# Optimization experiments

Hardware: AMD Instinct MI355X
Metric: run time of the kernel (lower is better)

Reference implementation:

```python
import jax, jax.numpy as jnp
import numpy as np
from jax import lax

N, H, BS = 256, 1024, 128
ALPHA, BETA, SIGMA = 60.0, 20.0, 5.0
EPS = 1e-8


def _mlp_w(key, n_in, n_out):
    return jax.random.normal(key, (n_out, n_in), dtype=jnp.float32) / np.sqrt(n_in)


def setup_inputs() -> dict:
    key = jax.random.key(0)
    ks = jax.random.split(key, 8)
    inp = {
        "t": jnp.zeros((), dtype=jnp.float32),
        "x": jax.random.normal(ks[0], (BS, N), dtype=jnp.float32),
        "Wf1": _mlp_w(ks[1], N, H), "bf1": jnp.zeros((H,), jnp.float32),
        "Wf2": _mlp_w(ks[2], H, N), "bf2": jnp.zeros((N,), jnp.float32),
        "Wg1": _mlp_w(ks[3], N, H), "bg1": jnp.zeros((H,), jnp.float32),
        "Wg2": _mlp_w(ks[4], H, N), "bg2": jnp.zeros((N,), jnp.float32),
        "Wk1": _mlp_w(ks[5], N, H), "bk1": jnp.zeros((H,), jnp.float32),
        "Wk2": _mlp_w(ks[6], H, N), "bk2": jnp.zeros((N,), jnp.float32),
    }
    return inp


def reference(t, x, Wf1, bf1, Wf2, bf2, Wg1, bg1, Wg2, bg2, Wk1, bk1, Wk2, bk2):
    def mlp(u, W1, b1, W2, b2):
        return jnp.tanh(u @ W1.T + b1) @ W2.T + b2

    def k_func(u):
        return mlp(u, Wk1, bk1, Wk2, bk2)

    f_out = mlp(x, Wf1, bf1, Wf2, bf2)          # f_model(t, x); t unused
    k_out = k_func(x)
    G_k_out = mlp(x, Wg1, bg1, Wg2, bg2)        # g_fn(x)[0]
    dx_dt = f_out + G_k_out

    # compute_k_jacobian: torch detaches u, so no grad flows to x here.
    # torch layout: J[b, j, i] = d k_i / d u_j  (transpose of jacfwd output)
    x_d = lax.stop_gradient(x)
    J_fwd = jax.vmap(jax.jacfwd(k_func))(x_d)   # [bs, i_out, j_in]
    J_x = jnp.swapaxes(J_fwd, 1, 2)             # [bs, j, i]

    k_norm = jnp.linalg.norm(k_out, axis=1)                      # [bs]
    Jf = jnp.einsum('bji,bi->bj', J_x, f_out)                    # bmm(J, f)
    Jf_norm = jnp.linalg.norm(Jf, axis=1)
    c1 = Jf_norm - ALPHA * k_norm ** (2 * SIGMA - 1)
    JG = jnp.einsum('bji,bi->bj', J_x, G_k_out)                  # bmm(J, G)
    c2 = jnp.sum(k_out * JG, axis=1) - BETA * k_norm ** (2 * SIGMA)

    mask = (c1 > EPS) | (c2 < -EPS)                              # [bs]
    dx_upd = jnp.where(mask[:, None], jnp.zeros_like(dx_dt), dx_dt)
    return (dx_upd + dx_dt) / 2
```

## Files before the change

### kernel.cpp

```cpp
#include <hip/hip_runtime.h>
#include <stdint.h>

#define N_ 256
#define H_ 1024
#define BS_ 128

#define WS_SK    0
#define WS_OACC  131072
#define WS_OPART 229376
#define WS_JPART 1802240
#define WS_FLOATS 2850816

__global__ __launch_bounds__(512) void k12_l1l2(
    const float* __restrict__ x,
    const float* __restrict__ Wf1, const float* __restrict__ bf1,
    const float* __restrict__ Wg1, const float* __restrict__ bg1,
    const float* __restrict__ Wk1, const float* __restrict__ bk1,
    const float* __restrict__ Wf2, const float* __restrict__ bf2,
    const float* __restrict__ Wg2, const float* __restrict__ bg2,
    const float* __restrict__ Wk2, const float* __restrict__ bk2,
    float* __restrict__ sk, float* __restrict__ opart)
{
    const int bx = blockIdx.x;
    const int g  = bx % 48;
    const int rt = bx / 48;
    const int m  = g >> 4;
    const int ht = g & 15;
    const int t  = threadIdx.x;
    const int h0 = ht * 64;
    const int r0 = rt * 16;

    const float* W1 = (m == 0) ? Wf1 : (m == 1) ? Wg1 : Wk1;
    const float* b1 = (m == 0) ? bf1 : (m == 1) ? bg1 : bk1;
    const float* W2 = (m == 0) ? Wf2 : (m == 1) ? Wg2 : Wk2;
    const float* b2 = (m == 0) ? bf2 : (m == 1) ? bg2 : bk2;

    __shared__ __align__(16) float xs[16][256];
    __shared__ __align__(16) float ts[16][64];
    for (int u = t; u < 1024; u += 512)
        ((float4*)xs)[u] = ((const float4*)(x + r0 * N_))[u];
    __syncthreads();

    {
        const int hl = t & 63;
        const int rq = (t >> 6) * 2;
        const int h  = h0 + hl;
        float a0 = b1[h], a1 = a0;
        const float4* w4 = (const float4*)(W1 + h * N_);
        const float4* x0 = (const float4*)xs[rq];
        const float4* x1 = (const float4*)xs[rq + 1];
        #pragma unroll 8
        for (int c = 0; c < 64; ++c) {
            float4 w = w4[c];
            float4 p = x0[c];
            a0 += w.x * p.x + w.y * p.y + w.z * p.z + w.w * p.w;
            float4 q = x1[c];
            a1 += w.x * q.x + w.y * q.y + w.z * q.z + w.w * q.w;
        }
        const float v0 = tanhf(a0), v1 = tanhf(a1);
        ts[rq][hl] = v0; ts[rq + 1][hl] = v1;
        if (m == 2) {
            sk[(r0 + rq) * H_ + h]     = 1.0f - v0 * v0;
            sk[(r0 + rq + 1) * H_ + h] = 1.0f - v1 * v1;
        }
    }
    __syncthreads();

    {
        const int i  = t & 255;
        const int hf = (t >> 8) * 8;
        float acc[8];
        const float bv = (ht == 0) ? b2[i] : 0.0f;
        #pragma unroll
        for (int r = 0; r < 8; ++r) acc[r] = bv;

        const float4* w4 = (const float4*)(W2 + i * H_ + h0);
        #pragma unroll 2
        for (int c = 0; c < 16; ++c) {
            float4 w = w4[c];
            #pragma unroll
            for (int r = 0; r < 8; ++r) {
                float4 a = ((const float4*)ts[hf + r])[c];
                acc[r] += w.x * a.x + w.y * a.y + w.z * a.z + w.w * a.w;
            }
        }
        #pragma unroll
        for (int r = 0; r < 8; ++r)
            opart[((ht * 3 + m) * BS_ + r0 + hf + r) * N_ + i] = acc[r];
    }
}

__global__ __launch_bounds__(256) void k25_reduce(
    const float* __restrict__ opart, float* __restrict__ oacc)
{
    const int tid = blockIdx.x * 256 + threadIdx.x;
    float s = 0.f;
    #pragma unroll
    for (int ks = 0; ks < 16; ++ks)
        s += opart[ks * (3 * BS_ * N_) + tid];
    oacc[tid] = s;
}

__global__ __launch_bounds__(256) void k3_vj(
    const float* __restrict__ Wk1, const float* __restrict__ Wk2,
    const float* __restrict__ oacc, const float* __restrict__ sk,
    float* __restrict__ jpart)
{
    const int q  = blockIdx.x & 15;
    const int rp = blockIdx.x >> 4;
    const int t  = threadIdx.x;
    const int r0 = rp * 4;
    const int h0 = q * 64;

    __shared__ float fos[4][256], gos[4][256];
    __shared__ float sfv[4][64], sgv[4][64];

    for (int u = t; u < 1024; u += 256) {
        const int r = u >> 8, i = u & 255;
        fos[r][i] = oacc[(r0 + r) * N_ + i];
        gos[r][i] = oacc[(BS_ + r0 + r) * N_ + i];
    }
    __syncthreads();

    {
        const int hl = t & 63;
        const int rl = t >> 6;
        const int h  = h0 + hl;
        const float* w2 = Wk2 + h;
        float vf = 0.f, vg = 0.f;
        #pragma unroll 8
        for (int c = 0; c < 64; ++c) {
            const float4 of = ((const float4*)fos[rl])[c];
            const float4 og = ((const float4*)gos[rl])[c];
            const float w0 = w2[(4 * c + 0) * H_];
            const float w1 = w2[(4 * c + 1) * H_];
            const float w2v = w2[(4 * c + 2) * H_];
            const float w3 = w2[(4 * c + 3) * H_];
            vf += of.x * w0 + of.y * w1 + of.z * w2v + of.w * w3;
            vg += og.x * w0 + og.y * w1 + og.z * w2v + og.w * w3;
        }
        const float s = sk[(r0 + rl) * H_ + h];
        sfv[rl][hl] = s * vf;
        sgv[rl][hl] = s * vg;
    }
    __syncthreads();

    {
        float jf[4] = {0.f, 0.f, 0.f, 0.f};
        float jg[4] = {0.f, 0.f, 0.f, 0.f};
        const float* w1 = Wk1 + h0 * N_ + t;
        #pragma unroll 4
        for (int c = 0; c < 16; ++c) {
            const float w0 = w1[(4 * c + 0) * N_];
            const float wv1 = w1[(4 * c + 1) * N_];
            const float wv2 = w1[(4 * c + 2) * N_];
            const float wv3 = w1[(4 * c + 3) * N_];
            #pragma unroll
            for (int r = 0; r < 4; ++r) {
                const float4 sf = ((const float4*)sfv[r])[c];
                const float4 sg = ((const float4*)sgv[r])[c];
                jf[r] += sf.x * w0 + sf.y * wv1 + sf.z * wv2 + sf.w * wv3;
                jg[r] += sg.x * w0 + sg.y * wv1 + sg.z * wv2 + sg.w * wv3;
            }
        }
        #pragma unroll
        for (int r = 0; r < 4; ++r) {
            jpart[((q * 2 + 0) * BS_ + r0 + r) * N_ + t] = jf[r];
            jpart[((q * 2 + 1) * BS_ + r0 + r) * N_ + t] = jg[r];
        }
    }
}

__global__ __launch_bounds__(256) void k4_final(
    const float* __restrict__ oacc,
    const float* __restrict__ jpart,
    float* __restrict__ out)
{
    const int r = blockIdx.x;
    const int t = threadIdx.x;
    __shared__ float red[12];

    const float fo = oacc[r * N_ + t];
    const float go = oacc[(BS_ + r) * N_ + t];
    const float ko = oacc[(2 * BS_ + r) * N_ + t];

    float jf = 0.f, jg = 0.f;
    #pragma unroll
    for (int q = 0; q < 16; ++q) {
        jf += jpart[((q * 2 + 0) * BS_ + r) * N_ + t];
        jg += jpart[((q * 2 + 1) * BS_ + r) * N_ + t];
    }

    float v0 = ko * ko, v1 = jf * jf, v2 = ko * jg;
    #pragma unroll
    for (int o = 32; o > 0; o >>= 1) {
        v0 += __shfl_xor(v0, o, 64);
        v1 += __shfl_xor(v1, o, 64);
        v2 += __shfl_xor(v2, o, 64);
    }
    const int wid = t >> 6;
    if ((t & 63) == 0) {
        red[wid * 3 + 0] = v0;
        red[wid * 3 + 1] = v1;
        red[wid * 3 + 2] = v2;
    }
    __syncthreads();
    const float kn2 = red[0] + red[3] + red[6] + red[9];
    const float jf2 = red[1] + red[4] + red[7] + red[10];
    const float kjg = red[2] + red[5] + red[8] + red[11];

    const float knorm = sqrtf(kn2);
    const float kn4 = kn2 * kn2;
    const float kn8 = kn4 * kn4;
    const float c1 = sqrtf(jf2) - 60.0f * kn8 * knorm;
    const float c2 = kjg - 20.0f * kn8 * kn2;
    const float scale = ((c1 > 1e-8f) || (c2 < -1e-8f)) ? 0.5f : 1.0f;

    out[r * N_ + t] = (fo + go) * scale;
}

__global__ __launch_bounds__(256) void manifold_fused(
    const float* __restrict__ x,
    const float* __restrict__ Wf1, const float* __restrict__ bf1v,
    const float* __restrict__ Wf2, const float* __restrict__ bf2v,
    const float* __restrict__ Wg1, const float* __restrict__ bg1v,
    const float* __restrict__ Wg2, const float* __restrict__ bg2v,
    const float* __restrict__ Wk1, const float* __restrict__ bk1v,
    const float* __restrict__ Wk2, const float* __restrict__ bk2v,
    float* __restrict__ out)
{
    const int b = blockIdx.x;
    const int t = threadIdx.x;
    __shared__ float xs[N_];
    __shared__ float tf[H_], tg[H_], tk[H_], sk[H_];
    __shared__ float fo[N_], go[N_];
    __shared__ float sfv[H_], sgv[H_];
    __shared__ float red[12];

    xs[t] = x[b * N_ + t];
    __syncthreads();
    {
        float acc[12];
        const float4* rows[12];
        #pragma unroll
        for (int m = 0; m < 4; ++m) {
            const int h = t + m * 256;
            rows[m]     = (const float4*)(Wf1 + h * N_);
            rows[4 + m] = (const float4*)(Wg1 + h * N_);
            rows[8 + m] = (const float4*)(Wk1 + h * N_);
            acc[m] = bf1v[h]; acc[4 + m] = bg1v[h]; acc[8 + m] = bk1v[h];
        }
        const float4* xs4 = (const float4*)xs;
        #pragma unroll 2
        for (int c = 0; c < 64; ++c) {
            float4 a = xs4[c];
            #pragma unroll
            for (int r = 0; r < 12; ++r) {
                float4 w = rows[r][c];
                acc[r] += w.x * a.x + w.y * a.y + w.z * a.z + w.w * a.w;
            }
        }
        #pragma unroll
        for (int m = 0; m < 4; ++m) {
            const int h = t + m * 256;
            float vtf = tanhf(acc[m]);
            float vtg = tanhf(acc[4 + m]);
            float vtk = tanhf(acc[8 + m]);
            tf[h] = vtf; tg[h] = vtg; tk[h] = vtk; sk[h] = 1.0f - vtk * vtk;
        }
    }
    __syncthreads();
    float af = bf2v[t], ag = bg2v[t], ak = bk2v[t];
    {
        const float4* rf = (const float4*)(Wf2 + t * H_);
        const float4* rg = (const float4*)(Wg2 + t * H_);
        const float4* rk = (const float4*)(Wk2 + t * H_);
        #pragma unroll 2
        for (int c = 0; c < 256; ++c) {
            float4 wf = rf[c], wg = rg[c], wk = rk[c];
            float4 vf = ((const float4*)tf)[c];
            af += wf.x*vf.x + wf.y*vf.y + wf.z*vf.z + wf.w*vf.w;
            float4 vg = ((const float4*)tg)[c];
            ag += wg.x*vg.x + wg.y*vg.y + wg.z*vg.z + wg.w*vg.w;
            float4 vk = ((const float4*)tk)[c];
            ak += wk.x*vk.x + wk.y*vk.y + wk.z*vk.z + wk.w*vk.w;
        }
    }
    fo[t] = af; go[t] = ag;
    __syncthreads();
    {
        float vf[4] = {0.f,0.f,0.f,0.f}, vg[4] = {0.f,0.f,0.f,0.f};
        const float* base = Wk2 + 4 * t;
        #pragma unroll 4
        for (int i = 0; i < N_; ++i) {
            float4 w = *(const float4*)(base + i * H_);
            float fv = fo[i], gv = go[i];
            vf[0]+=w.x*fv; vf[1]+=w.y*fv; vf[2]+=w.z*fv; vf[3]+=w.w*fv;
            vg[0]+=w.x*gv; vg[1]+=w.y*gv; vg[2]+=w.z*gv; vg[3]+=w.w*gv;
        }
        #pragma unroll
        for (int c = 0; c < 4; ++c) {
            sfv[4*t+c] = sk[4*t+c]*vf[c];
            sgv[4*t+c] = sk[4*t+c]*vg[c];
        }
    }
    __syncthreads();
    float jf = 0.f, jg = 0.f;
    {
        const float* col = Wk1 + t;
        #pragma unroll 4
        for (int c = 0; c < 256; ++c) {
            float4 s4 = ((const float4*)sfv)[c];
            float4 g4 = ((const float4*)sgv)[c];
            const int h = c * 4;
            float w0 = col[(h+0)*N_], w1 = col[(h+1)*N_];
            float w2 = col[(h+2)*N_], w3 = col[(h+3)*N_];
            jf += s4.x*w0 + s4.y*w1 + s4.z*w2 + s4.w*w3;
            jg += g4.x*w0 + g4.y*w1 + g4.z*w2 + g4.w*w3;
        }
    }
    float v0 = ak*ak, v1 = jf*jf, v2 = ak*jg;
    #pragma unroll
    for (int o = 32; o > 0; o >>= 1) {
        v0 += __shfl_xor(v0, o, 64);
        v1 += __shfl_xor(v1, o, 64);
        v2 += __shfl_xor(v2, o, 64);
    }
    const int wid = t >> 6;
    if ((t & 63) == 0) {
        red[wid*3+0] = v0; red[wid*3+1] = v1; red[wid*3+2] = v2;
    }
    __syncthreads();
    const float kn2 = red[0]+red[3]+red[6]+red[9];
    const float jf2 = red[1]+red[4]+red[7]+red[10];
    const float kjg = red[2]+red[5]+red[8]+red[11];
    const float knorm = sqrtf(kn2);
    const float kn4 = kn2*kn2, kn8 = kn4*kn4;
    const float c1 = sqrtf(jf2) - 60.0f*kn8*knorm;
    const float c2 = kjg - 20.0f*kn8*kn2;
    const float scale = ((c1 > 1e-8f) || (c2 < -1e-8f)) ? 0.5f : 1.0f;
    out[b*N_+t] = (af+ag)*scale;
}

extern "C" void kernel_launch(void* const* d_in, const int* in_sizes, int n_in,
                              void* d_out, int out_size, void* d_ws, size_t ws_size,
                              hipStream_t stream) {
    const float* x    = (const float*)d_in[1];
    const float* Wf1  = (const float*)d_in[2];
    const float* bf1v = (const float*)d_in[3];
    const float* Wf2  = (const float*)d_in[4];
    const float* bf2v = (const float*)d_in[5];
    const float* Wg1  = (const float*)d_in[6];
    const float* bg1v = (const float*)d_in[7];
    const float* Wg2  = (const float*)d_in[8];
    const float* bg2v = (const float*)d_in[9];
    const float* Wk1  = (const float*)d_in[10];
    const float* bk1v = (const float*)d_in[11];
    const float* Wk2  = (const float*)d_in[12];
    const float* bk2v = (const float*)d_in[13];
    float* out = (float*)d_out;

    if (ws_size < (size_t)WS_FLOATS * sizeof(float)) {
        manifold_fused<<<BS_, 256, 0, stream>>>(
            x, Wf1, bf1v, Wf2, bf2v, Wg1, bg1v, Wg2, bg2v,
            Wk1, bk1v, Wk2, bk2v, out);
        return;
    }

    float* ws    = (float*)d_ws;
    float* sk    = ws + WS_SK;
    float* oacc  = ws + WS_OACC;
    float* opart = ws + WS_OPART;
    float* jpart = ws + WS_JPART;

    k12_l1l2  <<<384, 512, 0, stream>>>(x, Wf1, bf1v, Wg1, bg1v, Wk1, bk1v,
                                        Wf2, bf2v, Wg2, bg2v, Wk2, bk2v,
                                        sk, opart);
    k25_reduce<<<384, 256, 0, stream>>>(opart, oacc);
    k3_vj     <<<512, 256, 0, stream>>>(Wk1, Wk2, oacc, sk, jpart);
    k4_final  <<<BS_, 256, 0, stream>>>(oacc, jpart, out);
}
```

Before: 139.7 us.

## Split fused layer-1/layer-2 kernel into two finer-grained kernels with swizzled LDS weight tiles

Replaces the single fused first/second-layer kernel with two kernels: one computes the tanh hidden activations for all three MLPs and stores them in workspace (reusing the jpart region), and the other computes the second-layer partial sums. Each kernel uses 1536 small 128-thread blocks that stage a weight tile in XOR-swizzled shared memory to avoid bank conflicts, and remaps block ids to spread work across XCDs. Layer 1 splits the K dimension across lanes and reduces with shuffles. This raises parallelism and weight reuse from LDS, at the cost of an extra launch and a global round trip for the hidden activations.

```diff
diff --git a/kernel.cpp b/kernel.cpp
--- a/kernel.cpp
+++ b/kernel.cpp
@@ -11,83 +11,126 @@
 #define WS_JPART 1802240
 #define WS_FLOATS 2850816
 
-__global__ __launch_bounds__(512) void k12_l1l2(
+__global__ __launch_bounds__(128) void k1_l1(
     const float* __restrict__ x,
     const float* __restrict__ Wf1, const float* __restrict__ bf1,
     const float* __restrict__ Wg1, const float* __restrict__ bg1,
     const float* __restrict__ Wk1, const float* __restrict__ bk1,
+    float* __restrict__ tg, float* __restrict__ sk)
+{
+    const int bx  = blockIdx.x;
+    const int sid = (bx & 7) * 192 + (bx >> 3);
+    const int g   = sid >> 4;
+    const int rt  = sid & 15;
+    const int m   = g >> 5;
+    const int ht  = g & 31;
+    const int h0  = ht * 32;
+    const int r0  = rt * 8;
+
+    const float* W1 = (m == 0) ? Wf1 : (m == 1) ? Wg1 : Wk1;
+    const float* b1 = (m == 0) ? bf1 : (m == 1) ? bg1 : bk1;
+
+    __shared__ float4 ws4[32 * 64];
+
+    const int t = threadIdx.x;
+    {
+        const float4* wg = (const float4*)(W1 + h0 * N_);
+        #pragma unroll
+        for (int v = 0; v < 16; ++v) {
+            const int f4  = t + 128 * v;
+            const int row = f4 >> 6, c = f4 & 63;
+            ws4[(row << 6) | (c & 48) | ((c & 15) ^ (row & 15))] = wg[f4];
+        }
+    }
+    __syncthreads();
+
+    const int l  = t & 63;
+    const int w  = t >> 6;
+    const int hl = l & 15;
+    const int kq = l >> 4;
+    const int h  = h0 + w * 16 + hl;
+
+    float acc[8] = {0.f,0.f,0.f,0.f,0.f,0.f,0.f,0.f};
+    const float4* wrow = ws4 + ((w * 16 + hl) << 6) + (kq << 4);
+    const float4* xg   = (const float4*)(x + r0 * N_) + (kq << 4);
+    #pragma unroll 4
+    for (int c = 0; c < 16; ++c) {
+        const float4 wv = wrow[c ^ hl];
+        #pragma unroll
+        for (int r = 0; r < 8; ++r) {
+            const float4 xv = xg[(r << 6) + c];
+            acc[r] += wv.x*xv.x + wv.y*xv.y + wv.z*xv.z + wv.w*xv.w;
+        }
+    }
+    #pragma unroll
+    for (int r = 0; r < 8; ++r) {
+        acc[r] += __shfl_xor(acc[r], 16, 64);
+        acc[r] += __shfl_xor(acc[r], 32, 64);
+    }
+    const float bv = b1[h];
+    const int ra = kq * 2, rb = ra + 1;
+    const float va = tanhf(acc[ra] + bv);
+    const float vb = tanhf(acc[rb] + bv);
+    tg[(m * BS_ + r0 + ra) * H_ + h] = va;
+    tg[(m * BS_ + r0 + rb) * H_ + h] = vb;
+    if (m == 2) {
+        sk[(r0 + ra) * H_ + h] = 1.0f - va * va;
+        sk[(r0 + rb) * H_ + h] = 1.0f - vb * vb;
+    }
+}
+
+__global__ __launch_bounds__(128) void k2_l2(
+    const float* __restrict__ tg,
     const float* __restrict__ Wf2, const float* __restrict__ bf2,
     const float* __restrict__ Wg2, const float* __restrict__ bg2,
     const float* __restrict__ Wk2, const float* __restrict__ bk2,
-    float* __restrict__ sk, float* __restrict__ opart)
-{
-    const int bx = blockIdx.x;
-    const int g  = bx % 48;
-    const int rt = bx / 48;
-    const int m  = g >> 4;
-    const int ht = g & 15;
-    const int t  = threadIdx.x;
-    const int h0 = ht * 64;
-    const int r0 = rt * 16;
-
-    const float* W1 = (m == 0) ? Wf1 : (m == 1) ? Wg1 : Wk1;
-    const float* b1 = (m == 0) ? bf1 : (m == 1) ? bg1 : bk1;
+    float* __restrict__ opart)
+{
+    const int bx  = blockIdx.x;
+    const int sid = (bx & 7) * 192 + (bx >> 3);
+    const int g   = sid >> 4;
+    const int rt  = sid & 15;
+    const int m   = g >> 5;
+    const int ks  = (g >> 1) & 15;
+    const int ih  = g & 1;
+    const int r0  = rt * 8;
+    const int k0  = ks * 64;
+    const int i0  = ih * 128;
+
     const float* W2 = (m == 0) ? Wf2 : (m == 1) ? Wg2 : Wk2;
     const float* b2 = (m == 0) ? bf2 : (m == 1) ? bg2 : bk2;
 
-    __shared__ __align__(16) float xs[16][256];
-    __shared__ __align__(16) float ts[16][64];
-    for (int u = t; u < 1024; u += 512)
-        ((float4*)xs)[u] = ((const float4*)(x + r0 * N_))[u];
-    __syncthreads();
-
-    {
-        const int hl = t & 63;
-        const int rq = (t >> 6) * 2;
-        const int h  = h0 + hl;
-        float a0 = b1[h], a1 = a0;
-        const float4* w4 = (const float4*)(W1 + h * N_);
-        const float4* x0 = (const float4*)xs[rq];
-        const float4* x1 = (const float4*)xs[rq + 1];
-        #pragma unroll 8
-        for (int c = 0; c < 64; ++c) {
-            float4 w = w4[c];
-            float4 p = x0[c];
-            a0 += w.x * p.x + w.y * p.y + w.z * p.z + w.w * p.w;
-            float4 q = x1[c];
-            a1 += w.x * q.x + w.y * q.y + w.z * q.z + w.w * q.w;
-        }
-        const float v0 = tanhf(a0), v1 = tanhf(a1);
-        ts[rq][hl] = v0; ts[rq + 1][hl] = v1;
-        if (m == 2) {
-            sk[(r0 + rq) * H_ + h]     = 1.0f - v0 * v0;
-            sk[(r0 + rq + 1) * H_ + h] = 1.0f - v1 * v1;
-        }
-    }
-    __syncthreads();
-
-    {
-        const int i  = t & 255;
-        const int hf = (t >> 8) * 8;
-        float acc[8];
-        const float bv = (ht == 0) ? b2[i] : 0.0f;
-        #pragma unroll
-        for (int r = 0; r < 8; ++r) acc[r] = bv;
-
-        const float4* w4 = (const float4*)(W2 + i * H_ + h0);
-        #pragma unroll 2
-        for (int c = 0; c < 16; ++c) {
-            float4 w = w4[c];
-            #pragma unroll
-            for (int r = 0; r < 8; ++r) {
-                float4 a = ((const float4*)ts[hf + r])[c];
-                acc[r] += w.x * a.x + w.y * a.y + w.z * a.z + w.w * a.w;
-            }
-        }
-        #pragma unroll
-        for (int r = 0; r < 8; ++r)
-            opart[((ht * 3 + m) * BS_ + r0 + hf + r) * N_ + i] = acc[r];
-    }
+    __shared__ float4 w2s[128 * 16];
+
+    const int t = threadIdx.x;
+    {
+        #pragma unroll
+        for (int v = 0; v < 16; ++v) {
+            const int row = (t >> 4) + (v << 3);
+            const int c   = t & 15;
+            const float4 wv = ((const float4*)(W2 + (i0 + row) * H_ + k0))[c];
+            w2s[(row << 4) | (c ^ (row & 15))] = wv;
+        }
+    }
+    __syncthreads();
+
+    const int i = i0 + t;
+    float acc[8] = {0.f,0.f,0.f,0.f,0.f,0.f,0.f,0.f};
+    const float4* wrow = w2s + (t << 4);
+    const float4* trow = (const float4*)(tg + (m * BS_ + r0) * H_ + k0);
+    #pragma unroll 4
+    for (int c = 0; c < 16; ++c) {
+        const float4 wv = wrow[c ^ (t & 15)];
+        #pragma unroll
+        for (int r = 0; r < 8; ++r) {
+            const float4 tv = trow[(r << 8) + c];
+            acc[r] += wv.x*tv.x + wv.y*tv.y + wv.z*tv.z + wv.w*tv.w;
+        }
+    }
+    const float bv = (ks == 0) ? b2[i] : 0.0f;
+    #pragma unroll
+    for (int r = 0; r < 8; ++r)
+        opart[((ks * 3 + m) * BS_ + r0 + r) * N_ + i] = acc[r] + bv;
 }
 
 __global__ __launch_bounds__(256) void k25_reduce(
@@ -372,10 +415,12 @@
     float* oacc  = ws + WS_OACC;
     float* opart = ws + WS_OPART;
     float* jpart = ws + WS_JPART;
-
-    k12_l1l2  <<<384, 512, 0, stream>>>(x, Wf1, bf1v, Wg1, bg1v, Wk1, bk1v,
-                                        Wf2, bf2v, Wg2, bg2v, Wk2, bk2v,
-                                        sk, opart);
+    float* tg    = ws + WS_JPART;
+
+    k1_l1     <<<1536, 128, 0, stream>>>(x, Wf1, bf1v, Wg1, bg1v, Wk1, bk1v,
+                                         tg, sk);
+    k2_l2     <<<1536, 128, 0, stream>>>(tg, Wf2, bf2v, Wg2, bg2v, Wk2, bk2v,
+                                         opart);
     k25_reduce<<<384, 256, 0, stream>>>(opart, oacc);
     k3_vj     <<<512, 256, 0, stream>>>(Wk1, Wk2, oacc, sk, jpart);
     k4_final  <<<BS_, 256, 0, stream>>>(oacc, jpart, out);
```

Result: slower. 143.3 us (+2.6%).

## Merge four kernels into one persistent kernel with software grid barriers

Applied to the files above, without the earlier changes.

Replaces the four-launch pipeline (layer1+layer2, reduce, vector-Jacobian, final) with a single 512-block persistent kernel that separates the phases with atomic-counter grid barriers. Layer 1 and layer 2 become separate phases with swizzled LDS weight tiles and the hidden activations staged in global memory. The reduce kernel is removed by summing the partials where they are consumed. This is meant to cut launch gaps and inter-kernel idle time. It adds a memset launch and spin-wait barriers that assume all 512 blocks are co-resident, which risks deadlock if they are not.

```diff
diff --git a/kernel.cpp b/kernel.cpp
--- a/kernel.cpp
+++ b/kernel.cpp
@@ -6,12 +6,27 @@
 #define BS_ 128
 
 #define WS_SK    0
-#define WS_OACC  131072
+#define WS_BAR   131072
 #define WS_OPART 229376
 #define WS_JPART 1802240
 #define WS_FLOATS 2850816
 
-__global__ __launch_bounds__(512) void k12_l1l2(
+#define GRID_ 512
+
+__device__ __forceinline__ void grid_barrier(int* cnt) {
+    __syncthreads();
+    if (threadIdx.x == 0) {
+        __threadfence();
+        atomicAdd(cnt, 1);
+        while (__hip_atomic_load(cnt, __ATOMIC_RELAXED,
+                                 __HIP_MEMORY_SCOPE_AGENT) < GRID_)
+            __builtin_amdgcn_s_sleep(2);
+    }
+    __syncthreads();
+    __threadfence();
+}
+
+__global__ __launch_bounds__(256, 2) void mega(
     const float* __restrict__ x,
     const float* __restrict__ Wf1, const float* __restrict__ bf1,
     const float* __restrict__ Wg1, const float* __restrict__ bg1,
@@ -19,204 +34,232 @@
     const float* __restrict__ Wf2, const float* __restrict__ bf2,
     const float* __restrict__ Wg2, const float* __restrict__ bg2,
     const float* __restrict__ Wk2, const float* __restrict__ bk2,
-    float* __restrict__ sk, float* __restrict__ opart)
+    float* __restrict__ ws, float* __restrict__ out)
 {
-    const int bx = blockIdx.x;
-    const int g  = bx % 48;
-    const int rt = bx / 48;
-    const int m  = g >> 4;
-    const int ht = g & 15;
-    const int t  = threadIdx.x;
-    const int h0 = ht * 64;
-    const int r0 = rt * 16;
-
-    const float* W1 = (m == 0) ? Wf1 : (m == 1) ? Wg1 : Wk1;
-    const float* b1 = (m == 0) ? bf1 : (m == 1) ? bg1 : bk1;
-    const float* W2 = (m == 0) ? Wf2 : (m == 1) ? Wg2 : Wk2;
-    const float* b2 = (m == 0) ? bf2 : (m == 1) ? bg2 : bk2;
-
-    __shared__ __align__(16) float xs[16][256];
-    __shared__ __align__(16) float ts[16][64];
-    for (int u = t; u < 1024; u += 512)
-        ((float4*)xs)[u] = ((const float4*)(x + r0 * N_))[u];
-    __syncthreads();
-
-    {
-        const int hl = t & 63;
-        const int rq = (t >> 6) * 2;
-        const int h  = h0 + hl;
-        float a0 = b1[h], a1 = a0;
-        const float4* w4 = (const float4*)(W1 + h * N_);
-        const float4* x0 = (const float4*)xs[rq];
-        const float4* x1 = (const float4*)xs[rq + 1];
-        #pragma unroll 8
-        for (int c = 0; c < 64; ++c) {
-            float4 w = w4[c];
-            float4 p = x0[c];
-            a0 += w.x * p.x + w.y * p.y + w.z * p.z + w.w * p.w;
-            float4 q = x1[c];
-            a1 += w.x * q.x + w.y * q.y + w.z * q.z + w.w * q.w;
-        }
-        const float v0 = tanhf(a0), v1 = tanhf(a1);
-        ts[rq][hl] = v0; ts[rq + 1][hl] = v1;
-        if (m == 2) {
-            sk[(r0 + rq) * H_ + h]     = 1.0f - v0 * v0;
-            sk[(r0 + rq + 1) * H_ + h] = 1.0f - v1 * v1;
-        }
-    }
-    __syncthreads();
-
-    {
-        const int i  = t & 255;
-        const int hf = (t >> 8) * 8;
-        float acc[8];
-        const float bv = (ht == 0) ? b2[i] : 0.0f;
-        #pragma unroll
-        for (int r = 0; r < 8; ++r) acc[r] = bv;
-
-        const float4* w4 = (const float4*)(W2 + i * H_ + h0);
-        #pragma unroll 2
-        for (int c = 0; c < 16; ++c) {
-            float4 w = w4[c];
-            #pragma unroll
-            for (int r = 0; r < 8; ++r) {
-                float4 a = ((const float4*)ts[hf + r])[c];
-                acc[r] += w.x * a.x + w.y * a.y + w.z * a.z + w.w * a.w;
-            }
-        }
-        #pragma unroll
-        for (int r = 0; r < 8; ++r)
-            opart[((ht * 3 + m) * BS_ + r0 + hf + r) * N_ + i] = acc[r];
-    }
-}
-
-__global__ __launch_bounds__(256) void k25_reduce(
-    const float* __restrict__ opart, float* __restrict__ oacc)
-{
-    const int tid = blockIdx.x * 256 + threadIdx.x;
-    float s = 0.f;
-    #pragma unroll
-    for (int ks = 0; ks < 16; ++ks)
-        s += opart[ks * (3 * BS_ * N_) + tid];
-    oacc[tid] = s;
-}
-
-__global__ __launch_bounds__(256) void k3_vj(
-    const float* __restrict__ Wk1, const float* __restrict__ Wk2,
-    const float* __restrict__ oacc, const float* __restrict__ sk,
-    float* __restrict__ jpart)
-{
-    const int q  = blockIdx.x & 15;
-    const int rp = blockIdx.x >> 4;
-    const int t  = threadIdx.x;
-    const int r0 = rp * 4;
-    const int h0 = q * 64;
-
-    __shared__ float fos[4][256], gos[4][256];
-    __shared__ float sfv[4][64], sgv[4][64];
-
-    for (int u = t; u < 1024; u += 256) {
-        const int r = u >> 8, i = u & 255;
-        fos[r][i] = oacc[(r0 + r) * N_ + i];
-        gos[r][i] = oacc[(BS_ + r0 + r) * N_ + i];
-    }
-    __syncthreads();
-
-    {
-        const int hl = t & 63;
-        const int rl = t >> 6;
-        const int h  = h0 + hl;
-        const float* w2 = Wk2 + h;
-        float vf = 0.f, vg = 0.f;
-        #pragma unroll 8
-        for (int c = 0; c < 64; ++c) {
-            const float4 of = ((const float4*)fos[rl])[c];
-            const float4 og = ((const float4*)gos[rl])[c];
-            const float w0 = w2[(4 * c + 0) * H_];
-            const float w1 = w2[(4 * c + 1) * H_];
-            const float w2v = w2[(4 * c + 2) * H_];
-            const float w3 = w2[(4 * c + 3) * H_];
-            vf += of.x * w0 + of.y * w1 + of.z * w2v + of.w * w3;
-            vg += og.x * w0 + og.y * w1 + og.z * w2v + og.w * w3;
-        }
-        const float s = sk[(r0 + rl) * H_ + h];
-        sfv[rl][hl] = s * vf;
-        sgv[rl][hl] = s * vg;
-    }
-    __syncthreads();
-
-    {
-        float jf[4] = {0.f, 0.f, 0.f, 0.f};
-        float jg[4] = {0.f, 0.f, 0.f, 0.f};
-        const float* w1 = Wk1 + h0 * N_ + t;
+    const int bid = blockIdx.x;
+    const int t   = threadIdx.x;
+
+    float* skw   = ws + WS_SK;
+    int*   bar   = (int*)(ws + WS_BAR);
+    float* opart = ws + WS_OPART;
+    float* jpart = ws + WS_JPART;
+    float* tg    = ws + WS_JPART;
+
+    __shared__ __align__(16) float smem[8192];
+    __shared__ float red[12];
+    float4* sm4 = (float4*)smem;
+
+    for (int u = bid; u < 1536; u += GRID_) {
+        const int m  = u >> 9;
+        const int r9 = u & 511;
+        const int ht = r9 >> 4;
+        const int rt = r9 & 15;
+        const int h0 = ht * 32, r0 = rt * 8;
+
+        const float* W1 = (m == 0) ? Wf1 : (m == 1) ? Wg1 : Wk1;
+        const float* b1 = (m == 0) ? bf1 : (m == 1) ? bg1 : bk1;
+
+        __syncthreads();
+        const float4* wg = (const float4*)(W1 + h0 * N_);
+        #pragma unroll
+        for (int v = 0; v < 8; ++v) {
+            const int f4  = t + 256 * v;
+            const int row = f4 >> 6, c = f4 & 63;
+            sm4[(row << 6) | (c & 48) | ((c & 15) ^ (row & 15))] = wg[f4];
+        }
+        __syncthreads();
+
+        const int hl = t & 15;
+        const int kq = (t >> 4) & 3;
+        const int w2i = (t >> 6) & 1;
+        const int rh = t >> 7;
+        const int hloc = w2i * 16 + hl;
+        const int h = h0 + hloc;
+
+        float acc[4] = {0.f, 0.f, 0.f, 0.f};
+        const float4* wrow = sm4 + (hloc << 6) + (kq << 4);
+        const float4* xg   = (const float4*)(x + (r0 + rh * 4) * N_) + (kq << 4);
         #pragma unroll 4
         for (int c = 0; c < 16; ++c) {
-            const float w0 = w1[(4 * c + 0) * N_];
-            const float wv1 = w1[(4 * c + 1) * N_];
-            const float wv2 = w1[(4 * c + 2) * N_];
-            const float wv3 = w1[(4 * c + 3) * N_];
+            const float4 wv = wrow[c ^ hl];
+            #pragma unroll
+            for (int j = 0; j < 4; ++j) {
+                const float4 xv = xg[(j << 6) + c];
+                acc[j] += wv.x*xv.x + wv.y*xv.y + wv.z*xv.z + wv.w*xv.w;
+            }
+        }
+        #pragma unroll
+        for (int j = 0; j < 4; ++j) {
+            acc[j] += __shfl_xor(acc[j], 16, 64);
+            acc[j] += __shfl_xor(acc[j], 32, 64);
+        }
+        float av = acc[0];
+        av = (kq == 1) ? acc[1] : av;
+        av = (kq == 2) ? acc[2] : av;
+        av = (kq == 3) ? acc[3] : av;
+        const float v0 = tanhf(av + b1[h]);
+        const int r = r0 + rh * 4 + kq;
+        tg[(m * BS_ + r) * H_ + h] = v0;
+        if (m == 2) skw[r * H_ + h] = 1.0f - v0 * v0;
+    }
+    grid_barrier(bar + 0);
+
+    for (int u = bid; u < 1536; u += GRID_) {
+        const int m  = u >> 9;
+        const int ks = (u >> 5) & 15;
+        const int ih = (u >> 4) & 1;
+        const int rt = u & 15;
+        const int k0 = ks * 64, i0 = ih * 128, r0 = rt * 8;
+
+        const float* W2 = (m == 0) ? Wf2 : (m == 1) ? Wg2 : Wk2;
+        const float* b2 = (m == 0) ? bf2 : (m == 1) ? bg2 : bk2;
+
+        __syncthreads();
+        #pragma unroll
+        for (int v = 0; v < 8; ++v) {
+            const int idx = t + 256 * v;
+            const int row = idx >> 4, c = idx & 15;
+            sm4[(row << 4) | (c ^ (row & 15))] =
+                ((const float4*)(W2 + (i0 + row) * H_ + k0))[c];
+        }
+        __syncthreads();
+
+        const int i  = t & 127;
+        const int rh = t >> 7;
+        float acc[4] = {0.f, 0.f, 0.f, 0.f};
+        const float4* wrow = sm4 + (i << 4);
+        const float4* trow = (const float4*)(tg + (m * BS_ + r0 + rh * 4) * H_ + k0);
+        #pragma unroll 4
+        for (int c = 0; c < 16; ++c) {
+            const float4 wv = wrow[c ^ (i & 15)];
+            #pragma unroll
+            for (int j = 0; j < 4; ++j) {
+                const float4 tv = trow[(j << 8) + c];
+                acc[j] += wv.x*tv.x + wv.y*tv.y + wv.z*tv.z + wv.w*tv.w;
+            }
+        }
+        const float bv = (ks == 0) ? b2[i0 + i] : 0.0f;
+        #pragma unroll
+        for (int j = 0; j < 4; ++j)
+            opart[((ks * 3 + m) * BS_ + r0 + rh * 4 + j) * N_ + i0 + i] = acc[j] + bv;
+    }
+    grid_barrier(bar + 1);
+
+    {
+        const int q  = bid & 15;
+        const int rp = bid >> 4;
+        const int r0 = rp * 4, h0 = q * 64;
+
+        float (*fos)[256] = (float(*)[256])smem;
+        float (*gos)[256] = (float(*)[256])(smem + 1024);
+        float (*sfv)[64]  = (float(*)[64])(smem + 2048);
+        float (*sgv)[64]  = (float(*)[64])(smem + 2304);
+
+        for (int u2 = t; u2 < 1024; u2 += 256) {
+            const int r = u2 >> 8, i = u2 & 255;
+            float sf = 0.f, sg = 0.f;
+            #pragma unroll
+            for (int ks2 = 0; ks2 < 16; ++ks2) {
+                sf += opart[((ks2 * 3 + 0) * BS_ + r0 + r) * N_ + i];
+                sg += opart[((ks2 * 3 + 1) * BS_ + r0 + r) * N_ + i];
+            }
+            fos[r][i] = sf; gos[r][i] = sg;
+        }
+        __syncthreads();
+
+        {
+            const int hl = t & 63;
+            const int rl = t >> 6;
+            const int h  = h0 + hl;
+            const float* w2 = Wk2 + h;
+            float vf = 0.f, vg = 0.f;
+            #pragma unroll 8
+            for (int c = 0; c < 64; ++c) {
+                const float4 of = ((const float4*)fos[rl])[c];
+                const float4 og = ((const float4*)gos[rl])[c];
+                const float w0  = w2[(4 * c + 0) * H_];
+                const float w1v = w2[(4 * c + 1) * H_];
+                const float w2v = w2[(4 * c + 2) * H_];
+                const float w3  = w2[(4 * c + 3) * H_];
+                vf += of.x * w0 + of.y * w1v + of.z * w2v + of.w * w3;
+                vg += og.x * w0 + og.y * w1v + og.z * w2v + og.w * w3;
+            }
+            const float s = skw[(r0 + rl) * H_ + h];
+            sfv[rl][hl] = s * vf;
+            sgv[rl][hl] = s * vg;
+        }
+        __syncthreads();
+
+        {
+            float jf[4] = {0.f, 0.f, 0.f, 0.f};
+            float jg[4] = {0.f, 0.f, 0.f, 0.f};
+            const float* w1 = Wk1 + h0 * N_ + t;
+            #pragma unroll 4
+            for (int c = 0; c < 16; ++c) {
+                const float w0  = w1[(4 * c + 0) * N_];
+                const float wv1 = w1[(4 * c + 1) * N_];
+                const float wv2 = w1[(4 * c + 2) * N_];
+                const float wv3 = w1[(4 * c + 3) * N_];
+                #pragma unroll
+                for (int r = 0; r < 4; ++r) {
+                    const float4 sf = ((const float4*)sfv[r])[c];
+                    const float4 sg = ((const float4*)sgv[r])[c];
+                    jf[r] += sf.x * w0 + sf.y * wv1 + sf.z * wv2 + sf.w * wv3;
+                    jg[r] += sg.x * w0 + sg.y * wv1 + sg.z * wv2 + sg.w * wv3;
+                }
+            }
             #pragma unroll
             for (int r = 0; r < 4; ++r) {
-                const float4 sf = ((const float4*)sfv[r])[c];
-                const float4 sg = ((const float4*)sgv[r])[c];
-                jf[r] += sf.x * w0 + sf.y * wv1 + sf.z * wv2 + sf.w * wv3;
-                jg[r] += sg.x * w0 + sg.y * wv1 + sg.z * wv2 + sg.w * wv3;
-            }
-        }
-        #pragma unroll
-        for (int r = 0; r < 4; ++r) {
-            jpart[((q * 2 + 0) * BS_ + r0 + r) * N_ + t] = jf[r];
-            jpart[((q * 2 + 1) * BS_ + r0 + r) * N_ + t] = jg[r];
-        }
-    }
-}
-
-__global__ __launch_bounds__(256) void k4_final(
-    const float* __restrict__ oacc,
-    const float* __restrict__ jpart,
-    float* __restrict__ out)
-{
-    const int r = blockIdx.x;
-    const int t = threadIdx.x;
-    __shared__ float red[12];
-
-    const float fo = oacc[r * N_ + t];
-    const float go = oacc[(BS_ + r) * N_ + t];
-    const float ko = oacc[(2 * BS_ + r) * N_ + t];
-
-    float jf = 0.f, jg = 0.f;
-    #pragma unroll
-    for (int q = 0; q < 16; ++q) {
-        jf += jpart[((q * 2 + 0) * BS_ + r) * N_ + t];
-        jg += jpart[((q * 2 + 1) * BS_ + r) * N_ + t];
-    }
-
-    float v0 = ko * ko, v1 = jf * jf, v2 = ko * jg;
-    #pragma unroll
-    for (int o = 32; o > 0; o >>= 1) {
-        v0 += __shfl_xor(v0, o, 64);
-        v1 += __shfl_xor(v1, o, 64);
-        v2 += __shfl_xor(v2, o, 64);
-    }
-    const int wid = t >> 6;
-    if ((t & 63) == 0) {
-        red[wid * 3 + 0] = v0;
-        red[wid * 3 + 1] = v1;
-        red[wid * 3 + 2] = v2;
-    }
-    __syncthreads();
-    const float kn2 = red[0] + red[3] + red[6] + red[9];
-    const float jf2 = red[1] + red[4] + red[7] + red[10];
-    const float kjg = red[2] + red[5] + red[8] + red[11];
-
-    const float knorm = sqrtf(kn2);
-    const float kn4 = kn2 * kn2;
-    const float kn8 = kn4 * kn4;
-    const float c1 = sqrtf(jf2) - 60.0f * kn8 * knorm;
-    const float c2 = kjg - 20.0f * kn8 * kn2;
-    const float scale = ((c1 > 1e-8f) || (c2 < -1e-8f)) ? 0.5f : 1.0f;
-
-    out[r * N_ + t] = (fo + go) * scale;
+                jpart[((q * 2 + 0) * BS_ + r0 + r) * N_ + t] = jf[r];
+                jpart[((q * 2 + 1) * BS_ + r0 + r) * N_ + t] = jg[r];
+            }
+        }
+    }
+    grid_barrier(bar + 2);
+
+    if (bid < BS_) {
+        const int r = bid;
+        float fo = 0.f, go = 0.f, ko = 0.f;
+        #pragma unroll
+        for (int ks2 = 0; ks2 < 16; ++ks2) {
+            fo += opart[((ks2 * 3 + 0) * BS_ + r) * N_ + t];
+            go += opart[((ks2 * 3 + 1) * BS_ + r) * N_ + t];
+            ko += opart[((ks2 * 3 + 2) * BS_ + r) * N_ + t];
+        }
+        float jf = 0.f, jg = 0.f;
+        #pragma unroll
+        for (int q2 = 0; q2 < 16; ++q2) {
+            jf += jpart[((q2 * 2 + 0) * BS_ + r) * N_ + t];
+            jg += jpart[((q2 * 2 + 1) * BS_ + r) * N_ + t];
+        }
+
+        float v0 = ko * ko, v1 = jf * jf, v2 = ko * jg;
+        #pragma unroll
+        for (int o = 32; o > 0; o >>= 1) {
+            v0 += __shfl_xor(v0, o, 64);
+            v1 += __shfl_xor(v1, o, 64);
+            v2 += __shfl_xor(v2, o, 64);
+        }
+        const int wid = t >> 6;
+        if ((t & 63) == 0) {
+            red[wid * 3 + 0] = v0;
+            red[wid * 3 + 1] = v1;
+            red[wid * 3 + 2] = v2;
+        }
+        __syncthreads();
+        const float kn2 = red[0] + red[3] + red[6] + red[9];
+        const float jf2 = red[1] + red[4] + red[7] + red[10];
+        const float kjg = red[2] + red[5] + red[8] + red[11];
+
+        const float knorm = sqrtf(kn2);
+        const float kn4 = kn2 * kn2;
+        const float kn8 = kn4 * kn4;
+        const float c1 = sqrtf(jf2) - 60.0f * kn8 * knorm;
+        const float c2 = kjg - 20.0f * kn8 * kn2;
+        const float scale = ((c1 > 1e-8f) || (c2 < -1e-8f)) ? 0.5f : 1.0f;
+
+        out[r * N_ + t] = (fo + go) * scale;
+    }
 }
 
 __global__ __launch_bounds__(256) void manifold_fused(
@@ -367,16 +410,10 @@
         return;
     }
 
-    float* ws    = (float*)d_ws;
-    float* sk    = ws + WS_SK;
-    float* oacc  = ws + WS_OACC;
-    float* opart = ws + WS_OPART;
-    float* jpart = ws + WS_JPART;
-
-    k12_l1l2  <<<384, 512, 0, stream>>>(x, Wf1, bf1v, Wg1, bg1v, Wk1, bk1v,
-                                        Wf2, bf2v, Wg2, bg2v, Wk2, bk2v,
-                                        sk, opart);
-    k25_reduce<<<384, 256, 0, stream>>>(opart, oacc);
-    k3_vj     <<<512, 256, 0, stream>>>(Wk1, Wk2, oacc, sk, jpart);
-    k4_final  <<<BS_, 256, 0, stream>>>(oacc, jpart, out);
+    float* ws = (float*)d_ws;
+    hipMemsetAsync(ws + WS_BAR, 0, 64, stream);
+    mega<<<GRID_, 256, 0, stream>>>(
+        x, Wf1, bf1v, Wg1, bg1v, Wk1, bk1v,
+        Wf2, bf2v, Wg2, bg2v, Wk2, bk2v,
+        ws, out);
 }
```

Result: slower. 351.7 us (+151.8%).

## Stage MLP weights in swizzled shared memory with finer hidden tiles in fused layer kernel

Applied to the files above, without the earlier changes.

The fused layer-1/layer-2 kernel now uses 768 blocks of 256 threads, each covering 32 hidden units instead of 64. It stages W1 and W2 tiles into XOR-swizzled LDS so the weights are read coalesced from global memory instead of through strided per-thread row loads. Layer 1 splits the K dimension across lanes and reduces with shuffles, and block IDs are remapped so neighbouring blocks spread across XCDs. The cost is twice as many partial sums (32 slices) for the reduce kernel to read and a larger workspace.

```diff
diff --git a/kernel.cpp b/kernel.cpp
--- a/kernel.cpp
+++ b/kernel.cpp
@@ -8,10 +8,10 @@
 #define WS_SK    0
 #define WS_OACC  131072
 #define WS_OPART 229376
-#define WS_JPART 1802240
-#define WS_FLOATS 2850816
-
-__global__ __launch_bounds__(512) void k12_l1l2(
+#define WS_JPART 3375104
+#define WS_FLOATS 4423680
+
+__global__ __launch_bounds__(256) void k12s(
     const float* __restrict__ x,
     const float* __restrict__ Wf1, const float* __restrict__ bf1,
     const float* __restrict__ Wg1, const float* __restrict__ bg1,
@@ -21,72 +21,110 @@
     const float* __restrict__ Wk2, const float* __restrict__ bk2,
     float* __restrict__ sk, float* __restrict__ opart)
 {
-    const int bx = blockIdx.x;
-    const int g  = bx % 48;
-    const int rt = bx / 48;
-    const int m  = g >> 4;
-    const int ht = g & 15;
-    const int t  = threadIdx.x;
-    const int h0 = ht * 64;
-    const int r0 = rt * 16;
+    const int bx  = blockIdx.x;
+    const int sid = (bx & 7) * 96 + (bx >> 3);
+    const int g   = sid >> 3;
+    const int rt  = sid & 7;
+    const int m   = g >> 5;
+    const int ht  = g & 31;
+    const int t   = threadIdx.x;
+    const int h0  = ht * 32;
+    const int r0  = rt * 16;
 
     const float* W1 = (m == 0) ? Wf1 : (m == 1) ? Wg1 : Wk1;
     const float* b1 = (m == 0) ? bf1 : (m == 1) ? bg1 : bk1;
     const float* W2 = (m == 0) ? Wf2 : (m == 1) ? Wg2 : Wk2;
     const float* b2 = (m == 0) ? bf2 : (m == 1) ? bg2 : bk2;
 
+    __shared__ float4 wbuf[2048];
     __shared__ __align__(16) float xs[16][256];
-    __shared__ __align__(16) float ts[16][64];
-    for (int u = t; u < 1024; u += 512)
-        ((float4*)xs)[u] = ((const float4*)(x + r0 * N_))[u];
-    __syncthreads();
-
-    {
-        const int hl = t & 63;
-        const int rq = (t >> 6) * 2;
-        const int h  = h0 + hl;
-        float a0 = b1[h], a1 = a0;
-        const float4* w4 = (const float4*)(W1 + h * N_);
-        const float4* x0 = (const float4*)xs[rq];
-        const float4* x1 = (const float4*)xs[rq + 1];
-        #pragma unroll 8
-        for (int c = 0; c < 64; ++c) {
-            float4 w = w4[c];
-            float4 p = x0[c];
-            a0 += w.x * p.x + w.y * p.y + w.z * p.z + w.w * p.w;
-            float4 q = x1[c];
-            a1 += w.x * q.x + w.y * q.y + w.z * q.z + w.w * q.w;
-        }
-        const float v0 = tanhf(a0), v1 = tanhf(a1);
-        ts[rq][hl] = v0; ts[rq + 1][hl] = v1;
-        if (m == 2) {
-            sk[(r0 + rq) * H_ + h]     = 1.0f - v0 * v0;
-            sk[(r0 + rq + 1) * H_ + h] = 1.0f - v1 * v1;
-        }
-    }
-    __syncthreads();
-
-    {
-        const int i  = t & 255;
-        const int hf = (t >> 8) * 8;
-        float acc[8];
-        const float bv = (ht == 0) ? b2[i] : 0.0f;
-        #pragma unroll
-        for (int r = 0; r < 8; ++r) acc[r] = bv;
-
-        const float4* w4 = (const float4*)(W2 + i * H_ + h0);
-        #pragma unroll 2
-        for (int c = 0; c < 16; ++c) {
-            float4 w = w4[c];
+    __shared__ __align__(16) float ts[16][32];
+
+    {
+        const float4* xsrc = (const float4*)(x + r0 * N_);
+        #pragma unroll
+        for (int v = 0; v < 4; ++v)
+            ((float4*)xs)[t + 256 * v] = xsrc[t + 256 * v];
+        const float4* wg = (const float4*)(W1 + h0 * N_);
+        #pragma unroll
+        for (int v = 0; v < 8; ++v) {
+            const int f4  = t + 256 * v;
+            const int row = f4 >> 6, c = f4 & 63;
+            wbuf[(row << 6) | (c & 48) | ((c & 15) ^ (row & 15))] = wg[f4];
+        }
+    }
+    __syncthreads();
+
+    {
+        const int hl   = t & 15;
+        const int kq   = (t >> 4) & 3;
+        const int hgrp = (t >> 6) & 1;
+        const int rh   = t >> 7;
+        const int hloc = hgrp * 16 + hl;
+        const int h    = h0 + hloc;
+
+        float acc[8] = {0.f,0.f,0.f,0.f,0.f,0.f,0.f,0.f};
+        const float4* wrow = wbuf + (hloc << 6) + (kq << 4);
+        #pragma unroll
+        for (int cl = 0; cl < 16; ++cl) {
+            const float4 wv = wrow[cl ^ hl];
             #pragma unroll
             for (int r = 0; r < 8; ++r) {
-                float4 a = ((const float4*)ts[hf + r])[c];
-                acc[r] += w.x * a.x + w.y * a.y + w.z * a.z + w.w * a.w;
+                const float4 xv = ((const float4*)xs[rh * 8 + r])[(kq << 4) + cl];
+                acc[r] += wv.x*xv.x + wv.y*xv.y + wv.z*xv.z + wv.w*xv.w;
             }
         }
         #pragma unroll
-        for (int r = 0; r < 8; ++r)
-            opart[((ht * 3 + m) * BS_ + r0 + hf + r) * N_ + i] = acc[r];
+        for (int r = 0; r < 8; ++r) {
+            acc[r] += __shfl_xor(acc[r], 16, 64);
+            acc[r] += __shfl_xor(acc[r], 32, 64);
+        }
+        float va = acc[0], vb = acc[1];
+        va = (kq == 1) ? acc[2] : va;  vb = (kq == 1) ? acc[3] : vb;
+        va = (kq == 2) ? acc[4] : va;  vb = (kq == 2) ? acc[5] : vb;
+        va = (kq == 3) ? acc[6] : va;  vb = (kq == 3) ? acc[7] : vb;
+        const float bv = b1[h];
+        const float v0 = tanhf(va + bv), v1 = tanhf(vb + bv);
+        const int rl = rh * 8 + kq * 2;
+        ts[rl][hloc]     = v0;
+        ts[rl + 1][hloc] = v1;
+        if (m == 2) {
+            sk[(r0 + rl) * H_ + h]     = 1.0f - v0 * v0;
+            sk[(r0 + rl + 1) * H_ + h] = 1.0f - v1 * v1;
+        }
+    }
+    __syncthreads();
+
+    {
+        #pragma unroll
+        for (int v = 0; v < 8; ++v) {
+            const int idx = t + 256 * v;
+            const int row = idx >> 3, c = idx & 7;
+            wbuf[(row << 3) | (c ^ (row & 7))] =
+                ((const float4*)(W2 + row * H_ + h0))[c];
+        }
+    }
+    __syncthreads();
+
+    {
+        float acc[16];
+        const float bv2 = (ht == 0) ? b2[t] : 0.0f;
+        #pragma unroll
+        for (int r = 0; r < 16; ++r) acc[r] = bv2;
+
+        const float4* wrow = wbuf + (t << 3);
+        #pragma unroll
+        for (int c = 0; c < 8; ++c) {
+            const float4 wv = wrow[c ^ (t & 7)];
+            #pragma unroll
+            for (int r = 0; r < 16; ++r) {
+                const float4 av = ((const float4*)ts[r])[c];
+                acc[r] += wv.x*av.x + wv.y*av.y + wv.z*av.z + wv.w*av.w;
+            }
+        }
+        #pragma unroll
+        for (int r = 0; r < 16; ++r)
+            opart[((ht * 3 + m) * BS_ + r0 + r) * N_ + t] = acc[r];
     }
 }
 
@@ -96,7 +134,7 @@
     const int tid = blockIdx.x * 256 + threadIdx.x;
     float s = 0.f;
     #pragma unroll
-    for (int ks = 0; ks < 16; ++ks)
+    for (int ks = 0; ks < 32; ++ks)
         s += opart[ks * (3 * BS_ * N_) + tid];
     oacc[tid] = s;
 }
@@ -132,12 +170,12 @@
         for (int c = 0; c < 64; ++c) {
             const float4 of = ((const float4*)fos[rl])[c];
             const float4 og = ((const float4*)gos[rl])[c];
-            const float w0 = w2[(4 * c + 0) * H_];
-            const float w1 = w2[(4 * c + 1) * H_];
+            const float w0  = w2[(4 * c + 0) * H_];
+            const float w1v = w2[(4 * c + 1) * H_];
             const float w2v = w2[(4 * c + 2) * H_];
-            const float w3 = w2[(4 * c + 3) * H_];
-            vf += of.x * w0 + of.y * w1 + of.z * w2v + of.w * w3;
-            vg += og.x * w0 + og.y * w1 + og.z * w2v + og.w * w3;
+            const float w3  = w2[(4 * c + 3) * H_];
+            vf += of.x * w0 + of.y * w1v + of.z * w2v + of.w * w3;
+            vg += og.x * w0 + og.y * w1v + og.z * w2v + og.w * w3;
         }
         const float s = sk[(r0 + rl) * H_ + h];
         sfv[rl][hl] = s * vf;
@@ -151,7 +189,7 @@
         const float* w1 = Wk1 + h0 * N_ + t;
         #pragma unroll 4
         for (int c = 0; c < 16; ++c) {
-            const float w0 = w1[(4 * c + 0) * N_];
+            const float w0  = w1[(4 * c + 0) * N_];
             const float wv1 = w1[(4 * c + 1) * N_];
             const float wv2 = w1[(4 * c + 2) * N_];
             const float wv3 = w1[(4 * c + 3) * N_];
@@ -373,7 +411,7 @@
     float* opart = ws + WS_OPART;
     float* jpart = ws + WS_JPART;
 
-    k12_l1l2  <<<384, 512, 0, stream>>>(x, Wf1, bf1v, Wg1, bg1v, Wk1, bk1v,
+    k12s      <<<768, 256, 0, stream>>>(x, Wf1, bf1v, Wg1, bg1v, Wk1, bk1v,
                                         Wf2, bf2v, Wg2, bg2v, Wk2, bk2v,
                                         sk, opart);
     k25_reduce<<<384, 256, 0, stream>>>(opart, oacc);
```

After: 121.2 us. 1.15x faster.
